# Performance work log

Measured on AMD Instinct MI355X. Metric: run time of the kernel, lower is better.

## Reference

```python
import jax, jax.numpy as jnp
import numpy as np

EMBED_DIM = 1024
NUM_HEADS = 16
ROTARY_THETA = 10000.0


def _rotate_half(t):
    d = t.shape[-1] // 2
    t1, t2 = t[..., :d], t[..., d:]
    return jnp.concatenate([-t2, t1], axis=-1)


def _rope_cos_sin(seq_len, head_dim, dtype):
    # inv_freq over even indices, standard RoPE
    inv_freq = 1.0 / (ROTARY_THETA ** (jnp.arange(0, head_dim, 2, dtype=jnp.float32) / head_dim))
    freqs = jnp.arange(seq_len, dtype=jnp.float32)[:, None] * inv_freq[None, :]  # (S, D/2)
    emb = jnp.concatenate([freqs, freqs], axis=-1)  # (S, D)
    # broadcast over (b, s, h, d)
    return jnp.cos(emb).astype(dtype)[None, :, None, :], jnp.sin(emb).astype(dtype)[None, :, None, :]


def setup_inputs() -> dict:
    key = jax.random.key(0)
    ks = jax.random.split(key, 4)
    B, S, E = 2, 2048, EMBED_DIM
    scale = 1.0 / np.sqrt(E)
    return {
        "x": jax.random.normal(ks[0], (B, S, E), dtype=jnp.float32),
        "attention_mask": jnp.zeros((B, 1, 1, S), dtype=jnp.float32),
        "Wq": jax.random.normal(ks[1], (E, E), dtype=jnp.float32) * scale,
        "bq": jnp.zeros((E,), dtype=jnp.float32),
        "Wk": jax.random.normal(ks[2], (E, E), dtype=jnp.float32) * scale,
        "bk": jnp.zeros((E,), dtype=jnp.float32),
        "Wv": jax.random.normal(ks[3], (E, E), dtype=jnp.float32) * scale,
        "bv": jnp.zeros((E,), dtype=jnp.float32),
    }


def reference(x, attention_mask, Wq, bq, Wk, bk, Wv, bv):
    B, S, E = x.shape
    H = NUM_HEADS
    D = E // H

    q = (x @ Wq + bq).reshape(B, S, H, D)
    k = (x @ Wk + bk).reshape(B, S, H, D)
    v = (x @ Wv + bv).reshape(B, S, H, D)

    cos, sin = _rope_cos_sin(S, D, q.dtype)
    q = q * cos + _rotate_half(q) * sin
    k = k * cos + _rotate_half(k) * sin

    # attention_mask: additive padding bias (b,1,1,k) broadcast over heads & queries
    scores = jnp.einsum("bqhd,bkhd->bhqk", q, k) / jnp.sqrt(jnp.asarray(D, dtype=q.dtype))
    scores = scores + attention_mask  # broadcasts to (b,h,q,k)
    attn = jax.nn.softmax(scores, axis=-1)
    out = jnp.einsum("bhqk,bkhd->bqhd", attn, v)
    return out.reshape(B, S, E)
```

## Files before the change

kernel.cpp:

```cpp
#include <hip/hip_runtime.h>

typedef __attribute__((ext_vector_type(8)))  short bf16x8;
typedef __attribute__((ext_vector_type(4)))  short s16x4;
typedef __attribute__((ext_vector_type(4)))  float f32x4;
typedef __attribute__((ext_vector_type(16))) float f32x16;
typedef __attribute__((ext_vector_type(4)))  unsigned u32x4;
typedef __attribute__((ext_vector_type(4)))  _Float16 f16x4;

#define B_  2
#define S_  2048
#define H_  16
#define D_  64
#define E_  1024
#define M_  (B_*S_)
#define L2E 1.44269504f

__device__ __forceinline__ unsigned short f2bf(float f){
  unsigned x = __builtin_bit_cast(unsigned, f);
  x += 0x7fffu + ((x >> 16) & 1u);
  return (unsigned short)(x >> 16);
}
__device__ __forceinline__ unsigned pk_bf16(float lo, float hi){
  unsigned short a = __builtin_bit_cast(unsigned short, (__bf16)lo);
  unsigned short b = __builtin_bit_cast(unsigned short, (__bf16)hi);
  return (unsigned)a | ((unsigned)b << 16);
}

#define GLD16(gp, lp) __builtin_amdgcn_global_load_lds( \
    (const __attribute__((address_space(1))) unsigned*)(gp), \
    (__attribute__((address_space(3))) unsigned*)(lp), 16, 0, 0)

__global__ __launch_bounds__(256) void k_cvt(const float* __restrict__ in, short* __restrict__ out,
                                             const float* __restrict__ mask,
                                             float* ct, float* st, float* maskC){
  int i = blockIdx.x*256 + threadIdx.x;
  if(i < S_*32){
    int s = i >> 5, f = i & 31;
    float invf = powf(10000.0f, -(float)f / 32.0f);
    float ph = (float)s * invf;
    ct[i] = cosf(ph);
    st[i] = sinf(ph);
    if(i < B_*S_) maskC[i] = fmaf(mask[i], L2E, -17.0f);
  }
  int j = i*4;
  float4 v = *(const float4*)(in + j);
  s16x4 o = { (short)f2bf(v.x), (short)f2bf(v.y), (short)f2bf(v.z), (short)f2bf(v.w) };
  *(s16x4*)(out + j) = o;
}

__global__ __launch_bounds__(256) void k_wt(const float* __restrict__ Wq, const float* __restrict__ Wk,
                                            const float* __restrict__ Wv, short* __restrict__ wt){
  const float* W = blockIdx.z==0 ? Wq : (blockIdx.z==1 ? Wk : Wv);
  short* out = wt + (size_t)blockIdx.z*E_*E_;
  __shared__ short tile[64][72];
  int nb = blockIdx.x*64, kb = blockIdx.y*64;
  int t = threadIdx.x;
  {
    int r = t>>2, c0 = (t&3)*16;
    const float* src = W + (size_t)(kb+r)*E_ + nb + c0;
    #pragma unroll
    for(int i=0;i<4;i++){
      float4 v = *(const float4*)(src + i*4);
      tile[r][c0+i*4+0] = (short)f2bf(v.x);
      tile[r][c0+i*4+1] = (short)f2bf(v.y);
      tile[r][c0+i*4+2] = (short)f2bf(v.z);
      tile[r][c0+i*4+3] = (short)f2bf(v.w);
    }
  }
  __syncthreads();
  {
    int n = t>>2, k0 = (t&3)*16;
    short* dst = out + (size_t)(nb+n)*E_ + kb + k0;
    bf16x8 o0, o1;
    #pragma unroll
    for(int i=0;i<8;i++){ o0[i] = tile[k0+i][n]; o1[i] = tile[k0+8+i][n]; }
    *(bf16x8*)dst = o0;
    *(bf16x8*)(dst+8) = o1;
  }
}

__global__ __launch_bounds__(256) void k_gemm(const short* __restrict__ A, const short* __restrict__ WT,
                                              const float* __restrict__ biasq, const float* __restrict__ biask,
                                              const float* __restrict__ biasv,
                                              short* __restrict__ oq, short* __restrict__ ok, short* __restrict__ ovt,
                                              const float* __restrict__ cost, const float* __restrict__ sint){
  const int z = blockIdx.z;
  const short* Bw = WT + (size_t)z*E_*E_;
  const float* bias = z==0 ? biasq : (z==1 ? biask : biasv);
  __shared__ short As[128*32];
  __shared__ short Bs[128*32];
  const int t = threadIdx.x, lane = t & 63, wid = t >> 6;
  const int mb = blockIdx.x*128, nb = blockIdx.y*128;
  const int wm = (wid>>1)*64, wn = (wid&1)*64;
  f32x4 acc[4][4] = {};
  for(int kt=0; kt<E_/32; kt++){
    __syncthreads();
    {
      int f0 = t, f1 = t + 256;
      GLD16(A  + (size_t)(mb + (f0>>2))*E_ + kt*32 + (f0&3)*8, &As[f0*8]);
      GLD16(A  + (size_t)(mb + (f1>>2))*E_ + kt*32 + (f1&3)*8, &As[f1*8]);
      GLD16(Bw + (size_t)(nb + (f0>>2))*E_ + kt*32 + (f0&3)*8, &Bs[f0*8]);
      GLD16(Bw + (size_t)(nb + (f1>>2))*E_ + kt*32 + (f1&3)*8, &Bs[f1*8]);
    }
    __syncthreads();
    bf16x8 af[4], bfv[4];
    #pragma unroll
    for(int mf=0; mf<4; mf++)
      af[mf] = *(const bf16x8*)&As[(wm + mf*16 + (lane&15))*32 + (lane>>4)*8];
    #pragma unroll
    for(int nf=0; nf<4; nf++)
      bfv[nf] = *(const bf16x8*)&Bs[(wn + nf*16 + (lane&15))*32 + (lane>>4)*8];
    #pragma unroll
    for(int mf=0; mf<4; mf++)
      #pragma unroll
      for(int nf=0; nf<4; nf++)
        acc[mf][nf] = __builtin_amdgcn_mfma_f32_16x16x32_bf16(af[mf], bfv[nf], acc[mf][nf], 0, 0, 0);
  }
  const int col16 = lane & 15, rg = lane >> 4;
  float bvs[4];
  #pragma unroll
  for(int nf=0; nf<4; nf++) bvs[nf] = bias[nb + wn + nf*16 + col16];
  if(z == 2){
    #pragma unroll
    for(int mf=0; mf<4; mf++){
      int row0 = mb + wm + mf*16 + rg*4;
      int bb2 = row0 >> 11, ss = row0 & (S_-1);
      #pragma unroll
      for(int nf=0; nf<4; nf++){
        int e = nb + wn + nf*16 + col16;
        int hh = e >> 6, dd = e & 63;
        s16x4 w = { (short)f2bf(acc[mf][nf][0]+bvs[nf]), (short)f2bf(acc[mf][nf][1]+bvs[nf]),
                    (short)f2bf(acc[mf][nf][2]+bvs[nf]), (short)f2bf(acc[mf][nf][3]+bvs[nf]) };
        *(s16x4*)(ovt + ((size_t)(bb2*H_+hh)*D_+dd)*S_ + ss) = w;
      }
    }
  } else {
    short* out = (z==0) ? oq : ok;
    const float qs = (z==0) ? (0.125f*L2E) : 1.0f;
    #pragma unroll
    for(int mf=0; mf<4; mf++)
      #pragma unroll
      for(int r=0; r<4; r++){
        int row = mb + wm + mf*16 + rg*4 + r;
        int srow = row & (S_-1);
        const float* cb = cost + (size_t)srow*32;
        const float* sb = sint + (size_t)srow*32;
        #pragma unroll
        for(int nf=0; nf<2; nf++){
          int d = nf*16 + col16;
          float c = cb[d], sn = sb[d];
          float x0 = acc[mf][nf][r]   + bvs[nf];
          float x1 = acc[mf][nf+2][r] + bvs[nf+2];
          out[(size_t)row*E_ + nb + wn + nf*16 + col16]     = (short)f2bf((x0*c - x1*sn)*qs);
          out[(size_t)row*E_ + nb + wn + (nf+2)*16 + col16] = (short)f2bf((x1*c + x0*sn)*qs);
        }
      }
  }
}

__global__ __launch_bounds__(256,4) void k_attn(
    const short* __restrict__ qg, const short* __restrict__ kg,
    const short* __restrict__ vtg, const float* __restrict__ maskC,
    float* __restrict__ o0g, _Float16* __restrict__ o1g, float* __restrict__ lpart){
  __shared__ short Ks[2][64*72];
  __shared__ short Vs[2][64*72];
  const int flat = blockIdx.x;
  const int v = flat >> 3;
  const int bh = (flat & 7)*4 + (v >> 5);
  const int inner = v & 31;
  const int qb = inner >> 1, sp = inner & 1;
  const int h = bh & 15, b = bh >> 4;
  const int tid = threadIdx.x, wid = tid>>6, lane = tid&63;
  const int l31 = lane & 31, hl = lane >> 5;
  const int qw = qb*128 + wid*32;
  const int rr = tid>>3, ch = tid&7;
  const int kb0 = sp*16;
  const int NT = 16;

  bf16x8 qf[4];
  {
    const short* qp = qg + ((size_t)(b*S_ + qw + l31)*H_ + h)*D_;
    #pragma unroll
    for(int dk=0; dk<4; dk++)
      qf[dk] = *(const bf16x8*)(qp + dk*16 + hl*8);
  }
  f32x16 O0 = {}, O1 = {};
  float l_run = 0.f;
  const float* mrow = maskC + (size_t)b*S_;

  bf16x8 ka, kc, va, vc;
#define LOADT(kb) { \
    const short* ks_ = kg + ((size_t)(b*S_ + (kb)*64 + rr)*H_ + h)*D_ + ch*8; \
    ka = *(const bf16x8*)ks_;  kc = *(const bf16x8*)(ks_ + 32*H_*D_); \
    const short* vs_ = vtg + ((size_t)(b*H_ + h)*D_ + rr)*S_ + (kb)*64 + ch*8; \
    va = *(const bf16x8*)vs_;  vc = *(const bf16x8*)(vs_ + 32*S_); }
#define WRITET(pp) { \
    *(bf16x8*)&Ks[pp][rr*72 + ch*8]      = ka; \
    *(bf16x8*)&Ks[pp][(rr+32)*72 + ch*8] = kc; \
    *(bf16x8*)&Vs[pp][rr*72 + ch*8]      = va; \
    *(bf16x8*)&Vs[pp][(rr+32)*72 + ch*8] = vc; }

  LOADT(kb0);
  WRITET(0);
  LOADT(kb0+1);
  asm volatile("s_waitcnt lgkmcnt(0)" ::: "memory");
  __builtin_amdgcn_s_barrier();

  int p = 0;
  for(int tt=0; tt<NT; tt++){
    f32x16 s0 = {}, s1 = {};
    __builtin_amdgcn_s_setprio(1);
    #pragma unroll
    for(int dk=0; dk<4; dk++){
      bf16x8 kf0 = *(const bf16x8*)&Ks[p][(l31)*72 + dk*16 + hl*8];
      bf16x8 kf1 = *(const bf16x8*)&Ks[p][(32+l31)*72 + dk*16 + hl*8];
      s0 = __builtin_amdgcn_mfma_f32_32x32x16_bf16(kf0, qf[dk], s0, 0,0,0);
      s1 = __builtin_amdgcn_mfma_f32_32x32x16_bf16(kf1, qf[dk], s1, 0,0,0);
    }
    __builtin_amdgcn_s_setprio(0);
    {
      const float* mt = mrow + (kb0+tt)*64 + hl*4;
      #pragma unroll
      for(int bb=0; bb<4; bb++){
        f32x4 mv0 = *(const f32x4*)(mt + bb*8);
        f32x4 mv1 = *(const f32x4*)(mt + 32 + bb*8);
        #pragma unroll
        for(int a=0; a<4; a++){ s0[bb*4+a] += mv0[a]; s1[bb*4+a] += mv1[a]; }
      }
    }
    #pragma unroll
    for(int i=0;i<16;i++) s0[i] = __builtin_amdgcn_exp2f(s0[i]);
    #pragma unroll
    for(int i=0;i<16;i++) s1[i] = __builtin_amdgcn_exp2f(s1[i]);
    float la=0.f, lb=0.f, lc=0.f, ld=0.f;
    #pragma unroll
    for(int i=0;i<4;i++){
      la += s0[i];   lb += s0[4+i];  lc += s0[8+i];  ld += s0[12+i];
      la += s1[i];   lb += s1[4+i];  lc += s1[8+i];  ld += s1[12+i];
    }
    float ls = (la+lb)+(lc+ld);
    ls += __shfl_xor(ls, 32);
    l_run += ls;

    unsigned w0a[8], w1a[8];
    #pragma unroll
    for(int c=0;c<8;c++){
      int base = (c&3)*4;
      float p0 = (c & 4) ? s1[base+0] : s0[base+0];
      float p1 = (c & 4) ? s1[base+1] : s0[base+1];
      float p2 = (c & 4) ? s1[base+2] : s0[base+2];
      float p3 = (c & 4) ? s1[base+3] : s0[base+3];
      w0a[c] = pk_bf16(p0, p1);
      w1a[c] = pk_bf16(p2, p3);
    }

    if(tt+1 < NT){
      WRITET(p^1);
      if(tt+2 < NT) LOADT(kb0+tt+2);
    }

    __builtin_amdgcn_s_setprio(1);
    #pragma unroll
    for(int ksl=0; ksl<4; ksl++){
      unsigned a0 = w0a[2*ksl], b0 = w0a[2*ksl+1];
      unsigned a1 = w1a[2*ksl], b1 = w1a[2*ksl+1];
      asm("v_permlane32_swap_b32 %0, %1" : "+v"(a0), "+v"(b0));
      asm("v_permlane32_swap_b32 %0, %1" : "+v"(a1), "+v"(b1));
      u32x4 pw = { a0, a1, b0, b1 };
      bf16x8 pf = __builtin_bit_cast(bf16x8, pw);
      bf16x8 vf0 = *(const bf16x8*)&Vs[p][(l31)*72 + ksl*16 + hl*8];
      bf16x8 vf1 = *(const bf16x8*)&Vs[p][(32+l31)*72 + ksl*16 + hl*8];
      O0 = __builtin_amdgcn_mfma_f32_32x32x16_bf16(pf, vf0, O0, 0,0,0);
      O1 = __builtin_amdgcn_mfma_f32_32x32x16_bf16(pf, vf1, O1, 0,0,0);
    }
    __builtin_amdgcn_s_setprio(0);
    asm volatile("s_waitcnt lgkmcnt(0)" ::: "memory");
    __builtin_amdgcn_s_barrier();
    p ^= 1;
  }
#undef LOADT
#undef WRITET

  if(sp == 0){
    #pragma unroll
    for(int bb=0; bb<4; bb++)
      #pragma unroll
      for(int a=0; a<4; a++){
        int qrow = qw + a + 8*bb + 4*hl;
        float* op = o0g + ((size_t)(b*S_ + qrow)*H_ + h)*D_;
        op[l31]      = O0[bb*4+a];
        op[32 + l31] = O1[bb*4+a];
      }
  } else {
    #pragma unroll
    for(int bb=0; bb<4; bb++)
      #pragma unroll
      for(int a=0; a<4; a++){
        int qrow = qw + a + 8*bb + 4*hl;
        _Float16* op = o1g + ((size_t)(b*S_ + qrow)*H_ + h)*D_;
        op[l31]      = (_Float16)O0[bb*4+a];
        op[32 + l31] = (_Float16)O1[bb*4+a];
      }
  }
  if(lane < 32)
    lpart[(size_t)sp*(M_*H_) + (size_t)(b*S_ + qw + l31)*H_ + h] = l_run;
}

__global__ __launch_bounds__(256) void k_comb(float* __restrict__ out, const _Float16* __restrict__ o1,
                                              const float* __restrict__ lpart){
  int i = blockIdx.x*256 + threadIdx.x;
  int idx = i*4;
  int lidx = idx >> 6;
  float linv = 1.f / (lpart[lidx] + lpart[M_*H_ + lidx]);
  f32x4 a = *(f32x4*)(out + idx);
  f16x4 bb = *(const f16x4*)(o1 + idx);
  f32x4 r = { (a[0] + (float)bb[0])*linv, (a[1] + (float)bb[1])*linv,
              (a[2] + (float)bb[2])*linv, (a[3] + (float)bb[3])*linv };
  *(f32x4*)(out + idx) = r;
}

extern "C" void kernel_launch(void* const* d_in, const int* in_sizes, int n_in,
                              void* d_out, int out_size, void* d_ws, size_t ws_size,
                              hipStream_t stream){
  (void)in_sizes; (void)n_in; (void)out_size; (void)ws_size;
  const float* x    = (const float*)d_in[0];
  const float* mask = (const float*)d_in[1];
  const float* Wq   = (const float*)d_in[2];
  const float* bq   = (const float*)d_in[3];
  const float* Wk   = (const float*)d_in[4];
  const float* bk   = (const float*)d_in[5];
  const float* Wv   = (const float*)d_in[6];
  const float* bv   = (const float*)d_in[7];
  float* out = (float*)d_out;
  char* ws = (char*)d_ws;
  float* cost  = (float*)(ws);
  float* sint  = (float*)(ws + (256u<<10));
  float* maskC = (float*)(ws + (512u<<10));
  float* lpart = (float*)(ws + (768u<<10));
  short* xb    = (short*)(ws + (2u<<20));
  short* wt    = (short*)(ws + (10u<<20));
  short* qb    = (short*)(ws + (16u<<20));
  short* kb    = (short*)(ws + (24u<<20));
  short* vtb   = (short*)(ws + (32u<<20));
  _Float16* o1 = (_Float16*)xb;

  k_cvt<<<dim3(4096), dim3(256), 0, stream>>>(x, xb, mask, cost, sint, maskC);
  k_wt<<<dim3(16,16,3), dim3(256), 0, stream>>>(Wq, Wk, Wv, wt);
  k_gemm<<<dim3(32,8,3), dim3(256), 0, stream>>>(xb, wt, bq, bk, bv, qb, kb, vtb, cost, sint);
  k_attn<<<dim3(1024), dim3(256), 0, stream>>>(qb, kb, vtb, maskC, out, o1, lpart);
  k_comb<<<dim3(4096), dim3(256), 0, stream>>>(out, o1, lpart);
}
```

Measured before the change: 118.5 us.

## Fuse prep kernels and merge split-KV combine into attention via atomic flags

Merges the input conversion and weight transpose kernels into one launch, and removes the separate combine kernel. Each attention block now bumps an atomic counter per (batch, head, query block). The second of the two split-KV blocks to finish reads its partner's partial output and normalizer and writes the final normalized result. This removes two kernel launches and a full pass over the output, at the cost of fences, an atomic per block and some tail imbalance for the finishing block.

```diff
diff --git a/kernel.cpp b/kernel.cpp
--- a/kernel.cpp
+++ b/kernel.cpp
@@ -5,7 +5,6 @@
 typedef __attribute__((ext_vector_type(4)))  float f32x4;
 typedef __attribute__((ext_vector_type(16))) float f32x16;
 typedef __attribute__((ext_vector_type(4)))  unsigned u32x4;
-typedef __attribute__((ext_vector_type(4)))  _Float16 f16x4;
 
 #define B_  2
 #define S_  2048
@@ -13,6 +12,7 @@
 #define D_  64
 #define E_  1024
 #define M_  (B_*S_)
+#define NH_ (M_*H_)
 #define L2E 1.44269504f
 
 __device__ __forceinline__ unsigned short f2bf(float f){
@@ -30,52 +30,57 @@
     (const __attribute__((address_space(1))) unsigned*)(gp), \
     (__attribute__((address_space(3))) unsigned*)(lp), 16, 0, 0)
 
-__global__ __launch_bounds__(256) void k_cvt(const float* __restrict__ in, short* __restrict__ out,
-                                             const float* __restrict__ mask,
-                                             float* ct, float* st, float* maskC){
-  int i = blockIdx.x*256 + threadIdx.x;
-  if(i < S_*32){
-    int s = i >> 5, f = i & 31;
-    float invf = powf(10000.0f, -(float)f / 32.0f);
-    float ph = (float)s * invf;
-    ct[i] = cosf(ph);
-    st[i] = sinf(ph);
-    if(i < B_*S_) maskC[i] = fmaf(mask[i], L2E, -17.0f);
-  }
-  int j = i*4;
-  float4 v = *(const float4*)(in + j);
-  s16x4 o = { (short)f2bf(v.x), (short)f2bf(v.y), (short)f2bf(v.z), (short)f2bf(v.w) };
-  *(s16x4*)(out + j) = o;
-}
-
-__global__ __launch_bounds__(256) void k_wt(const float* __restrict__ Wq, const float* __restrict__ Wk,
-                                            const float* __restrict__ Wv, short* __restrict__ wt){
-  const float* W = blockIdx.z==0 ? Wq : (blockIdx.z==1 ? Wk : Wv);
-  short* out = wt + (size_t)blockIdx.z*E_*E_;
-  __shared__ short tile[64][72];
-  int nb = blockIdx.x*64, kb = blockIdx.y*64;
-  int t = threadIdx.x;
-  {
-    int r = t>>2, c0 = (t&3)*16;
-    const float* src = W + (size_t)(kb+r)*E_ + nb + c0;
-    #pragma unroll
-    for(int i=0;i<4;i++){
-      float4 v = *(const float4*)(src + i*4);
-      tile[r][c0+i*4+0] = (short)f2bf(v.x);
-      tile[r][c0+i*4+1] = (short)f2bf(v.y);
-      tile[r][c0+i*4+2] = (short)f2bf(v.z);
-      tile[r][c0+i*4+3] = (short)f2bf(v.w);
-    }
-  }
-  __syncthreads();
-  {
-    int n = t>>2, k0 = (t&3)*16;
-    short* dst = out + (size_t)(nb+n)*E_ + kb + k0;
-    bf16x8 o0, o1;
-    #pragma unroll
-    for(int i=0;i<8;i++){ o0[i] = tile[k0+i][n]; o1[i] = tile[k0+8+i][n]; }
-    *(bf16x8*)dst = o0;
-    *(bf16x8*)(dst+8) = o1;
+__global__ __launch_bounds__(256) void k_prep(const float* __restrict__ in, short* __restrict__ out,
+                                              const float* __restrict__ mask,
+                                              float* ct, float* st, float* maskC, int* flags,
+                                              const float* __restrict__ Wq, const float* __restrict__ Wk,
+                                              const float* __restrict__ Wv, short* __restrict__ wt){
+  const int bx = blockIdx.x;
+  if(bx < 4096){
+    int i = bx*256 + threadIdx.x;
+    if(i < S_*32){
+      int s = i >> 5, f = i & 31;
+      float invf = powf(10000.0f, -(float)f / 32.0f);
+      float ph = (float)s * invf;
+      ct[i] = cosf(ph);
+      st[i] = sinf(ph);
+      if(i < B_*S_) maskC[i] = fmaf(mask[i], L2E, -17.0f);
+      if(i < B_*H_*16) flags[i] = 0;
+    }
+    int j = i*4;
+    float4 v = *(const float4*)(in + j);
+    s16x4 o = { (short)f2bf(v.x), (short)f2bf(v.y), (short)f2bf(v.z), (short)f2bf(v.w) };
+    *(s16x4*)(out + j) = o;
+  } else {
+    int w = bx - 4096;
+    int z = w >> 8, r = w & 255;
+    const float* W = z==0 ? Wq : (z==1 ? Wk : Wv);
+    short* outw = wt + (size_t)z*E_*E_;
+    __shared__ short tile[64][72];
+    int nb = (r & 15)*64, kb = (r >> 4)*64;
+    int t = threadIdx.x;
+    {
+      int rr = t>>2, c0 = (t&3)*16;
+      const float* src = W + (size_t)(kb+rr)*E_ + nb + c0;
+      #pragma unroll
+      for(int i=0;i<4;i++){
+        float4 v = *(const float4*)(src + i*4);
+        tile[rr][c0+i*4+0] = (short)f2bf(v.x);
+        tile[rr][c0+i*4+1] = (short)f2bf(v.y);
+        tile[rr][c0+i*4+2] = (short)f2bf(v.z);
+        tile[rr][c0+i*4+3] = (short)f2bf(v.w);
+      }
+    }
+    __syncthreads();
+    {
+      int n = t>>2, k0 = (t&3)*16;
+      short* dst = outw + (size_t)(nb+n)*E_ + kb + k0;
+      bf16x8 o0, o1;
+      #pragma unroll
+      for(int i=0;i<8;i++){ o0[i] = tile[k0+i][n]; o1[i] = tile[k0+8+i][n]; }
+      *(bf16x8*)dst = o0;
+      *(bf16x8*)(dst+8) = o1;
+    }
   }
 }
 
@@ -161,7 +166,8 @@
 __global__ __launch_bounds__(256,4) void k_attn(
     const short* __restrict__ qg, const short* __restrict__ kg,
     const short* __restrict__ vtg, const float* __restrict__ maskC,
-    float* __restrict__ o0g, _Float16* __restrict__ o1g, float* __restrict__ lpart){
+    float* __restrict__ o0g, _Float16* __restrict__ o1g, float* __restrict__ lpart,
+    int* __restrict__ flags){
   __shared__ short Ks[2][64*72];
   __shared__ short Vs[2][64*72];
   const int flat = blockIdx.x;
@@ -303,20 +309,35 @@
       }
   }
   if(lane < 32)
-    lpart[(size_t)sp*(M_*H_) + (size_t)(b*S_ + qw + l31)*H_ + h] = l_run;
-}
-
-__global__ __launch_bounds__(256) void k_comb(float* __restrict__ out, const _Float16* __restrict__ o1,
-                                              const float* __restrict__ lpart){
-  int i = blockIdx.x*256 + threadIdx.x;
-  int idx = i*4;
-  int lidx = idx >> 6;
-  float linv = 1.f / (lpart[lidx] + lpart[M_*H_ + lidx]);
-  f32x4 a = *(f32x4*)(out + idx);
-  f16x4 bb = *(const f16x4*)(o1 + idx);
-  f32x4 r = { (a[0] + (float)bb[0])*linv, (a[1] + (float)bb[1])*linv,
-              (a[2] + (float)bb[2])*linv, (a[3] + (float)bb[3])*linv };
-  *(f32x4*)(out + idx) = r;
+    lpart[(size_t)sp*NH_ + (size_t)(b*S_ + qw + l31)*H_ + h] = l_run;
+
+  __threadfence();
+  __shared__ int s_old;
+  __syncthreads();
+  if(tid == 0) s_old = atomicAdd(&flags[(b*H_ + h)*16 + qb], 1);
+  __syncthreads();
+  if(s_old == 1){
+    __threadfence();
+    #pragma unroll
+    for(int bb=0; bb<4; bb++)
+      #pragma unroll
+      for(int a=0; a<4; a++){
+        int qrow = qw + a + 8*bb + 4*hl;
+        size_t lidx = (size_t)(b*S_ + qrow)*H_ + h;
+        size_t base = lidx*D_;
+        float linv = 1.f / (lpart[lidx] + lpart[NH_ + lidx]);
+        float p0a, p0b, p1a, p1b;
+        if(sp == 0){
+          p0a = O0[bb*4+a];                  p0b = O1[bb*4+a];
+          p1a = (float)o1g[base + l31];      p1b = (float)o1g[base + 32 + l31];
+        } else {
+          p0a = o0g[base + l31];             p0b = o0g[base + 32 + l31];
+          p1a = (float)(_Float16)O0[bb*4+a]; p1b = (float)(_Float16)O1[bb*4+a];
+        }
+        o0g[base + l31]      = (p0a + p1a) * linv;
+        o0g[base + 32 + l31] = (p0b + p1b) * linv;
+      }
+  }
 }
 
 extern "C" void kernel_launch(void* const* d_in, const int* in_sizes, int n_in,
@@ -337,6 +358,7 @@
   float* sint  = (float*)(ws + (256u<<10));
   float* maskC = (float*)(ws + (512u<<10));
   float* lpart = (float*)(ws + (768u<<10));
+  int*   flags = (int*)(ws + (1280u<<10));
   short* xb    = (short*)(ws + (2u<<20));
   short* wt    = (short*)(ws + (10u<<20));
   short* qb    = (short*)(ws + (16u<<20));
@@ -344,9 +366,8 @@
   short* vtb   = (short*)(ws + (32u<<20));
   _Float16* o1 = (_Float16*)xb;
 
-  k_cvt<<<dim3(4096), dim3(256), 0, stream>>>(x, xb, mask, cost, sint, maskC);
-  k_wt<<<dim3(16,16,3), dim3(256), 0, stream>>>(Wq, Wk, Wv, wt);
+  k_prep<<<dim3(4096+768), dim3(256), 0, stream>>>(x, xb, mask, cost, sint, maskC, flags,
+                                                   Wq, Wk, Wv, wt);
   k_gemm<<<dim3(32,8,3), dim3(256), 0, stream>>>(xb, wt, bq, bk, bv, qb, kb, vtb, cost, sint);
-  k_attn<<<dim3(1024), dim3(256), 0, stream>>>(qb, kb, vtb, maskC, out, o1, lpart);
-  k_comb<<<dim3(4096), dim3(256), 0, stream>>>(out, o1, lpart);
-}
+  k_attn<<<dim3(1024), dim3(256), 0, stream>>>(qb, kb, vtb, maskC, out, o1, lpart, flags);
+}
```

Result: slower. 311.4 us (+162.8%).
